# Kernel tuning notes

Measured on AMD Instinct MI355X. Metric: run time of the kernel, lower is better.

Reference implementation:

```python
import jax, jax.numpy as jnp
import numpy as np

GAMMA = 0.99
N_CODES = 1024  # module hardcodes self.N = 2**10

def setup_inputs() -> dict:
    key = jax.random.key(0)
    k1, k2, k3, k4 = jax.random.split(key, 4)
    B, D, S = 16, 256, 2048
    N_q = 8
    return {
        "data_object": jax.random.normal(k1, (B, D, S), dtype=jnp.float32),
        "codebooks": jax.random.normal(k2, (N_q, N_CODES, D), dtype=jnp.float32),
        "N_i": jax.random.uniform(k3, (N_q, N_CODES), dtype=jnp.float32),
        "m_i": jax.random.normal(k4, (N_q, N_CODES, D), dtype=jnp.float32),
    }

def reference(data_object, codebooks, N_i, m_i):
    # data_object: [b, D, s] -> y: [b, s, D]
    b, D, s = data_object.shape
    y = jnp.transpose(data_object, (0, 2, 1))

    def stage(carry, xs):
        residual, cur_y = carry          # [b, s, D] each
        W, Ni, mi = xs                   # [N, D], [N], [N, D]
        flat = residual.reshape(-1, D)   # [b*s, D]
        d2 = (jnp.sum(flat * flat, axis=-1, keepdims=True)
              + jnp.sum(W * W, axis=-1)[None, :]
              - 2.0 * flat @ W.T)
        idx = jnp.argmin(d2, axis=-1)    # [b*s]
        Q = W[idx].reshape(residual.shape)
        # EMA codebook statistics (bincount + index_add as segment sums)
        counts = jax.ops.segment_sum(jnp.ones(idx.shape, flat.dtype), idx, num_segments=N_CODES)
        vec = jax.ops.segment_sum(flat, idx, num_segments=N_CODES)
        new_N = Ni * GAMMA + counts * (1.0 - GAMMA)
        new_m = mi * GAMMA + vec * (1.0 - GAMMA)
        new_W = new_m / jnp.clip(new_N, 1e-8)[:, None]
        return (residual - Q, cur_y + Q), (idx.reshape(b, s), new_N, new_m, new_W)

    init = (y, jnp.zeros_like(y))
    (residual, cur_y), (indices, new_N, new_m, new_W) = jax.lax.scan(
        stage, init, (codebooks, N_i, m_i))

    # straight-through estimator + commitment loss
    logits = y + jax.lax.stop_gradient(cur_y - y)       # [b, s, D]
    commitment_loss = jnp.mean((jax.lax.stop_gradient(cur_y) - y) ** 2)
    logits = jnp.transpose(logits, (0, 2, 1))           # back to [b, D, s]
    return logits, commitment_loss, indices, new_N, new_m, new_W
```

## Files before the change

### kernel.cpp

```cpp
#include <hip/hip_runtime.h>
#include <hip/hip_bf16.h>


using f16   = _Float16;
using f16x4 = __attribute__((ext_vector_type(4))) _Float16;
using f16x8 = __attribute__((ext_vector_type(8))) _Float16;
using f32x4 = __attribute__((ext_vector_type(4))) float;

#define GAMMA_F 0.99f
#define OMG_F   0.01f
#define LO_SCALE 1024.0f
#define LO_INV   (1.0f/1024.0f)

__global__ void sentinel_kernel(float* out, float v){
  if (threadIdx.x == 0 && blockIdx.x == 0) out[0] = v;
}

__global__ __launch_bounds__(64) void rownorm_kernel(const float* __restrict__ X,
                                                     float* __restrict__ out, int rows){
  int r = blockIdx.x;
  if (r >= rows) return;
  int l = threadIdx.x;
  const float* x = X + (size_t)r * 256;
  float s = 0.f;
  #pragma unroll
  for (int i = 0; i < 4; i++){ float v = x[l + i*64]; s += v*v; }
  #pragma unroll
  for (int o = 32; o > 0; o >>= 1) s += __shfl_down(s, o, 64);
  if (l == 0) out[r] = s;
}

__global__ __launch_bounds__(64) void wsplit_kernel(const float* __restrict__ W,
                                                    f16* __restrict__ frag){
  int blk = blockIdx.x;
  int lane = threadIdx.x;
  int code = (blk >> 3 << 4) + (lane & 15);
  int k0   = (blk & 7)*32 + (lane >> 4)*8;
  const float* src = W + (size_t)code * 256 + k0;
  float4 a = *(const float4*)(src);
  float4 b = *(const float4*)(src + 4);
  float x[8] = {a.x,a.y,a.z,a.w, b.x,b.y,b.z,b.w};
  f16x8 h8, l8;
  #pragma unroll
  for (int i = 0; i < 8; i++){
    f16 h = (f16)x[i];
    h8[i] = h;
    l8[i] = (f16)((x[i] - (float)h) * LO_SCALE);
  }
  f16* dst = frag + (size_t)blk * 1024 + lane*8;
  *(f16x8*)dst         = h8;
  *(f16x8*)(dst + 512) = l8;
}

__global__ __launch_bounds__(256) void init_kernel(const float* __restrict__ data,
                                                   f16* __restrict__ AH, f16* __restrict__ AL,
                                                   float* __restrict__ rnorm){
  __shared__ float rs[32][257];
  __shared__ float nrmp[32][8];
  int blk = blockIdx.x, b = blk >> 6, s0 = (blk & 63) * 32;
  int tid = threadIdx.x, c = tid & 31, g = tid >> 5;
  const float* dptr = data + (size_t)b * 524288 + s0;
  float np_ = 0.f;
  #pragma unroll 8
  for (int dd = 0; dd < 32; ++dd){
    int d = g*32 + dd;
    float x = dptr[(size_t)d * 2048 + c];
    rs[c][d] = x;
    np_ += x*x;
  }
  nrmp[c][g] = np_;
  __syncthreads();
  if (tid < 32){
    float s = 0.f;
    #pragma unroll
    for (int gg = 0; gg < 8; ++gg) s += nrmp[tid][gg];
    rnorm[blk*32 + tid] = s;
  }
  int r0 = blk*32;
  int c2 = tid >> 3, k0 = (tid & 7) * 32;
  #pragma unroll
  for (int jc = 0; jc < 4; ++jc){
    f16x8 h8, l8;
    #pragma unroll
    for (int j = 0; j < 8; ++j){
      float x = rs[c2][k0 + jc*8 + j];
      f16 h = (f16)x;
      h8[j] = h;
      l8[j] = (f16)((x - (float)h) * LO_SCALE);
    }
    size_t off = (size_t)(r0 + c2) * 256 + k0 + jc*8;
    *(f16x8*)(AH + off) = h8;
    *(f16x8*)(AL + off) = l8;
  }
}

__global__ __launch_bounds__(256) void out4init_kernel(const float* __restrict__ mi,
                                                       float* __restrict__ out4){
  int e4 = blockIdx.x*256 + threadIdx.x;
  float4 v = ((const float4*)mi)[e4];
  v.x *= GAMMA_F; v.y *= GAMMA_F; v.z *= GAMMA_F; v.w *= GAMMA_F;
  ((float4*)out4)[e4] = v;
}

__global__ __launch_bounds__(256, 2) void dist_kernel(
    const f16* __restrict__ AH, const f16* __restrict__ AL,
    const f16* __restrict__ whl, const float* __restrict__ wnorm,
    const float* __restrict__ rnorm, float* __restrict__ pv,
    unsigned short* __restrict__ pi, int q)
{
  __shared__ f16 Bs[2][8192];
  const int tid = threadIdx.x;
  const int lane = tid & 63;
  const int w = tid >> 6;
  const int rb = blockIdx.x, cs = blockIdx.y;
  const int rlo = lane & 15, kg = lane >> 4;
  const int T0 = rb*8 + w*2;

  f16x8 aH[2][8], aL[2][8];
  #pragma unroll
  for (int rt = 0; rt < 2; ++rt)
    #pragma unroll
    for (int kf = 0; kf < 8; ++kf){
      size_t off = (size_t)((T0+rt)*16 + rlo) * 256 + kf*32 + kg*8;
      aH[rt][kf] = *(const f16x8*)(AH + off);
      aL[rt][kf] = *(const f16x8*)(AL + off);
    }
  float rn[2][4];
  #pragma unroll
  for (int rt = 0; rt < 2; ++rt)
    #pragma unroll
    for (int i = 0; i < 4; ++i)
      rn[rt][i] = rnorm[(T0+rt)*16 + kg*4 + i];

  const f16* wb = whl + (size_t)q * 64 * 8192;
  const float* wn = wnorm + (q << 10);
  const int ct0 = cs * 16;

  float bestv[8]; int besti[8];
  #pragma unroll
  for (int r8 = 0; r8 < 8; ++r8){ bestv[r8] = 3.4e38f; besti[r8] = 0; }

  {
    const f16* src = wb + (size_t)ct0 * 8192;
    f16x8 st[4];
    #pragma unroll
    for (int j = 0; j < 4; ++j) st[j] = *(const f16x8*)(src + tid*8 + j*2048);
    #pragma unroll
    for (int j = 0; j < 4; ++j) *(f16x8*)(&Bs[0][0] + tid*8 + j*2048) = st[j];
  }

  for (int it = 0; it < 16; ++it){
    int ct = ct0 + it;
    __syncthreads();
    f16x8 nx[4];
    if (it < 15){
      const f16* src = wb + (size_t)(ct+1) * 8192;
      #pragma unroll
      for (int j = 0; j < 4; ++j) nx[j] = *(const f16x8*)(src + tid*8 + j*2048);
    }
    const f16* bb = &Bs[it & 1][0];
    f32x4 hh[2], cr[2];
    #pragma unroll
    for (int rt = 0; rt < 2; ++rt){ hh[rt] = (f32x4)0.0f; cr[rt] = (f32x4)0.0f; }
    #pragma unroll
    for (int kf = 0; kf < 8; ++kf){
      f16x8 bh = *(const f16x8*)(bb + kf*1024 + lane*8);
      f16x8 bl = *(const f16x8*)(bb + kf*1024 + 512 + lane*8);
      hh[0] = __builtin_amdgcn_mfma_f32_16x16x32_f16(aH[0][kf], bh, hh[0], 0,0,0);
      cr[0] = __builtin_amdgcn_mfma_f32_16x16x32_f16(aH[0][kf], bl, cr[0], 0,0,0);
      cr[0] = __builtin_amdgcn_mfma_f32_16x16x32_f16(aL[0][kf], bh, cr[0], 0,0,0);
      hh[1] = __builtin_amdgcn_mfma_f32_16x16x32_f16(aH[1][kf], bh, hh[1], 0,0,0);
      cr[1] = __builtin_amdgcn_mfma_f32_16x16x32_f16(aH[1][kf], bl, cr[1], 0,0,0);
      cr[1] = __builtin_amdgcn_mfma_f32_16x16x32_f16(aL[1][kf], bh, cr[1], 0,0,0);
    }
    {
      int code = (ct << 4) + rlo;
      float wnc = wn[code];
      #pragma unroll
      for (int rt = 0; rt < 2; ++rt)
        #pragma unroll
        for (int i = 0; i < 4; ++i){
          float dot = hh[rt][i] + cr[rt][i] * LO_INV;
          float d2 = (rn[rt][i] + wnc) - 2.0f * dot;
          int r8 = rt*4 + i;
          if (d2 < bestv[r8] || (d2 == bestv[r8] && code < besti[r8])){
            bestv[r8] = d2; besti[r8] = code;
          }
        }
    }
    if (it < 15){
      #pragma unroll
      for (int j = 0; j < 4; ++j) *(f16x8*)(&Bs[(it+1) & 1][0] + tid*8 + j*2048) = nx[j];
    }
  }

  #pragma unroll
  for (int off = 1; off <= 8; off <<= 1){
    #pragma unroll
    for (int r8 = 0; r8 < 8; ++r8){
      float ov = __shfl_xor(bestv[r8], off, 16);
      int   oi = __shfl_xor(besti[r8], off, 16);
      if (ov < bestv[r8] || (ov == bestv[r8] && oi < besti[r8])){
        bestv[r8] = ov; besti[r8] = oi;
      }
    }
  }
  if (rlo == 0){
    #pragma unroll
    for (int r8 = 0; r8 < 8; ++r8){
      int rt = r8 >> 2, i = r8 & 3;
      int grow = (T0 + rt)*16 + kg*4 + i;
      pv[cs*32768 + grow] = bestv[r8];
      pi[cs*32768 + grow] = (unsigned short)besti[r8];
    }
  }
}

__global__ __launch_bounds__(256) void combine_kernel(
    const float* __restrict__ pv, const unsigned short* __restrict__ pi,
    float* __restrict__ out2q, unsigned short* __restrict__ blockhist){
  __shared__ int h[1024];
  int tid = threadIdx.x, b = blockIdx.x;
  #pragma unroll
  for (int i = 0; i < 4; ++i) h[tid + 256*i] = 0;
  __syncthreads();
  #pragma unroll
  for (int j = 0; j < 4; ++j){
    int row = b*1024 + tid + 256*j;
    float bv = pv[row]; int bi = pi[row];
    #pragma unroll
    for (int cs = 1; cs < 4; ++cs){
      float v = pv[cs*32768 + row];
      int  ii = pi[cs*32768 + row];
      if (v < bv){ bv = v; bi = ii; }
    }
    out2q[row] = (float)bi;
    atomicAdd(&h[bi], 1);
  }
  __syncthreads();
  #pragma unroll
  for (int i = 0; i < 4; ++i)
    blockhist[b*1024 + tid + 256*i] = (unsigned short)h[tid + 256*i];
}

__global__ __launch_bounds__(256) void scan_kernel(unsigned short* __restrict__ blockhist,
                                                   const float* __restrict__ Ni,
                                                   float* __restrict__ out3, int q){
  __shared__ int wtot[4];
  int tid = threadIdx.x, lane = tid & 63, w = tid >> 6;
  ushort4* bh4 = (ushort4*)blockhist;
  int tx=0, ty=0, tz=0, tw=0;
  for (int b = 0; b < 32; ++b){
    ushort4 h = bh4[b*256 + tid];
    tx += h.x; ty += h.y; tz += h.z; tw += h.w;
  }
  int s = tx + ty + tz + tw;
  int v = s;
  #pragma unroll
  for (int d = 1; d < 64; d <<= 1){
    int o = __shfl_up(v, d, 64);
    if (lane >= d) v += o;
  }
  if (lane == 63) wtot[w] = v;
  __syncthreads();
  int woff = 0;
  #pragma unroll
  for (int ww = 0; ww < 4; ++ww) if (ww < w) woff += wtot[ww];
  int base = woff + v - s;
  const int qb = q << 10;
  out3[qb + tid*4+0] = Ni[qb + tid*4+0]*GAMMA_F + (float)tx*OMG_F;
  out3[qb + tid*4+1] = Ni[qb + tid*4+1]*GAMMA_F + (float)ty*OMG_F;
  out3[qb + tid*4+2] = Ni[qb + tid*4+2]*GAMMA_F + (float)tz*OMG_F;
  out3[qb + tid*4+3] = Ni[qb + tid*4+3]*GAMMA_F + (float)tw*OMG_F;
  int r0 = base, r1 = base + tx, r2 = r1 + ty, r3 = r2 + tz;
  for (int b = 0; b < 32; ++b){
    ushort4 h = bh4[b*256 + tid];
    ushort4 st; st.x = (unsigned short)r0; st.y = (unsigned short)r1;
    st.z = (unsigned short)r2; st.w = (unsigned short)r3;
    bh4[b*256 + tid] = st;
    r0 += h.x; r1 += h.y; r2 += h.z; r3 += h.w;
  }
}

__global__ __launch_bounds__(256) void scatter_kernel(const float* __restrict__ out2q,
                                                      const unsigned short* __restrict__ blockhist,
                                                      unsigned short* __restrict__ rowlist){
  __shared__ int cur[1024];
  int tid = threadIdx.x, b = blockIdx.x;
  #pragma unroll
  for (int i = 0; i < 4; ++i) cur[tid + 256*i] = blockhist[b*1024 + tid + 256*i];
  __syncthreads();
  #pragma unroll
  for (int j = 0; j < 4; ++j){
    int row = b*1024 + tid + 256*j;
    int c = (int)out2q[row];
    int pos = atomicAdd(&cur[c], 1);
    rowlist[pos] = (unsigned short)row;
  }
}

__global__ __launch_bounds__(64) void update_kernel(
    f16* __restrict__ AH, f16* __restrict__ AL,
    const unsigned short* __restrict__ rowlist, const float* __restrict__ out2q,
    const float* __restrict__ codebooks, float* __restrict__ out4,
    float* __restrict__ rnorm, int q)
{
  const int lane = threadIdx.x;
  const int s0 = blockIdx.x * 16;
  int myrow = 0, mycode = 0;
  if (lane < 16){
    myrow = rowlist[s0 + lane];
    mycode = (int)out2q[myrow];
  }
  float vs[4] = {0.f, 0.f, 0.f, 0.f};
  float Wk[4] = {0.f, 0.f, 0.f, 0.f};
  int prev = -1;
  for (int s = 0; s < 16; ++s){
    int row  = __shfl(myrow, s, 64);
    int code = __shfl(mycode, s, 64);
    if (code != prev){
      if (prev >= 0){
        float* dst = out4 + (((size_t)q << 10) + prev)*256 + lane*4;
        #pragma unroll
        for (int t = 0; t < 4; ++t) atomicAdd(dst + t, vs[t] * OMG_F);
      }
      float4 wv = *(const float4*)&codebooks[(((size_t)q << 10) + code)*256 + lane*4];
      Wk[0] = wv.x; Wk[1] = wv.y; Wk[2] = wv.z; Wk[3] = wv.w;
      vs[0] = vs[1] = vs[2] = vs[3] = 0.f;
      prev = code;
    }
    size_t base = (size_t)row * 256 + lane*4;
    f16x4 h4 = *(const f16x4*)(AH + base);
    f16x4 l4 = *(const f16x4*)(AL + base);
    f16x4 nh, nl;
    float p = 0.f;
    #pragma unroll
    for (int t = 0; t < 4; ++t){
      float rj = (float)h4[t] + (float)l4[t] * LO_INV;
      vs[t] += rj;
      float rn_ = rj - Wk[t];
      f16 hh = (f16)rn_;
      nh[t] = hh;
      nl[t] = (f16)((rn_ - (float)hh) * LO_SCALE);
      p += rn_ * rn_;
    }
    *(f16x4*)(AH + base) = nh;
    *(f16x4*)(AL + base) = nl;
    #pragma unroll
    for (int o = 32; o > 0; o >>= 1) p += __shfl_down(p, o, 64);
    if (lane == 0) rnorm[row] = p;
  }
  if (prev >= 0){
    float* dst = out4 + (((size_t)q << 10) + prev)*256 + lane*4;
    #pragma unroll
    for (int t = 0; t < 4; ++t) atomicAdd(dst + t, vs[t] * OMG_F);
  }
}

__global__ __launch_bounds__(256) void logits_loss_kernel(
    const float* __restrict__ data, const f16* __restrict__ AH, const f16* __restrict__ AL,
    float* __restrict__ out0, float* __restrict__ out1)
{
  __shared__ float rs[32][257];
  int blk = blockIdx.x, b = blk >> 6, s0 = (blk & 63) * 32;
  int tid = threadIdx.x;
  int r0 = blk*32;
  int c2 = tid >> 3, k0 = (tid & 7) * 32;
  #pragma unroll
  for (int jc = 0; jc < 4; ++jc){
    size_t off = (size_t)(r0 + c2) * 256 + k0 + jc*8;
    f16x8 h8 = *(const f16x8*)(AH + off);
    f16x8 l8 = *(const f16x8*)(AL + off);
    #pragma unroll
    for (int j = 0; j < 8; ++j)
      rs[c2][k0 + jc*8 + j] = (float)h8[j] + (float)l8[j] * LO_INV;
  }
  __syncthreads();
  int c = tid & 31, g = tid >> 5;
  const float* dptr = data + (size_t)b * 524288 + s0;
  float* optr = out0 + (size_t)b * 524288 + s0;
  float lsum = 0.f;
  #pragma unroll 8
  for (int dd = 0; dd < 32; ++dd){
    int d = g*32 + dd;
    float r = rs[c][d];
    lsum += r*r;
    optr[(size_t)d * 2048 + c] = dptr[(size_t)d * 2048 + c] - r;
  }
  #pragma unroll
  for (int o = 32; o > 0; o >>= 1) lsum += __shfl_down(lsum, o, 64);
  if ((tid & 63) == 0) atomicAdd(out1, lsum * (1.0f / 8388608.0f));
}

__global__ __launch_bounds__(256) void out5_kernel(const float* __restrict__ out4,
                                                   const float* __restrict__ out3,
                                                   float* __restrict__ out5){
  int e4 = blockIdx.x*256 + threadIdx.x;
  float Nn = fmaxf(out3[e4 >> 6], 1e-8f);
  float4 v = ((const float4*)out4)[e4];
  v.x /= Nn; v.y /= Nn; v.z /= Nn; v.w /= Nn;
  ((float4*)out5)[e4] = v;
}

extern "C" void kernel_launch(void* const* d_in, const int* in_sizes, int n_in,
                              void* d_out, int out_size, void* d_ws, size_t ws_size,
                              hipStream_t stream){
  float* out = (float*)d_out;

  const float* data = nullptr; const float* codebooks = nullptr;
  const float* Ni = nullptr;   const float* mi = nullptr;
  for (int i = 0; i < n_in; ++i){
    if      (in_sizes[i] == 8388608) data = (const float*)d_in[i];
    else if (in_sizes[i] == 8192)    Ni   = (const float*)d_in[i];
    else if (in_sizes[i] == 2097152){
      if (!codebooks) codebooks = (const float*)d_in[i];
      else            mi        = (const float*)d_in[i];
    }
  }
  if (!data || !codebooks || !Ni || !mi){
    sentinel_kernel<<<1, 64, 0, stream>>>(out, 6666.0f);
    return;
  }

  const size_t ws_need = 43122688ull;
  if (ws_size < ws_need){
    sentinel_kernel<<<1, 64, 0, stream>>>(out, 7777.0f);
    return;
  }
  f16*   AH     = (f16*)d_ws;
  f16*   AL     = AH + 8388608;
  f16*   whl    = AL + 8388608;
  float* wnormb = (float*)(whl + 4194304);
  float* rnorm  = wnormb + 8192;
  unsigned short* blockhist = (unsigned short*)(rnorm + 32768);
  unsigned short* rowlist   = blockhist + 32768;
  float* pv     = (float*)(rowlist + 32768);
  unsigned short* pi = (unsigned short*)(pv + 131072);

  float* out0 = out;
  float* out1 = out0 + 8388608;
  float* out2 = out1 + 1;
  float* out3 = out2 + 262144;
  float* out4 = out3 + 8192;
  float* out5 = out4 + 2097152;

  hipMemsetAsync(out1, 0, sizeof(float), stream);

  wsplit_kernel<<<dim3(4096), 64, 0, stream>>>(codebooks, whl);
  rownorm_kernel<<<dim3(8192), 64, 0, stream>>>(codebooks, wnormb, 8192);
  init_kernel<<<dim3(1024), 256, 0, stream>>>(data, AH, AL, rnorm);
  out4init_kernel<<<dim3(2048), 256, 0, stream>>>(mi, out4);

  for (int q = 0; q < 8; ++q){
    float* out2q = out2 + (size_t)q * 32768;
    dist_kernel<<<dim3(256, 4), 256, 0, stream>>>(AH, AL, whl, wnormb, rnorm, pv, pi, q);
    combine_kernel<<<dim3(32), 256, 0, stream>>>(pv, pi, out2q, blockhist);
    scan_kernel<<<dim3(1), 256, 0, stream>>>(blockhist, Ni, out3, q);
    scatter_kernel<<<dim3(32), 256, 0, stream>>>(out2q, blockhist, rowlist);
    update_kernel<<<dim3(2048), 64, 0, stream>>>(AH, AL, rowlist, out2q,
                                                 codebooks, out4, rnorm, q);
  }

  logits_loss_kernel<<<dim3(1024), 256, 0, stream>>>(data, AH, AL, out0, out1);
  out5_kernel<<<dim3(2048), 256, 0, stream>>>(out4, out3, out5);
}
```

Before: 867.0 us.

## Load codebook low-half fragments from global into registers and prefetch update rows

In the distance kernel, only the high-half codebook fragments are now staged in shared memory, which halves the LDS footprint. The low-half fragments are loaded straight from global memory into registers on each tile iteration. In the update kernel, the next row's residual halves are loaded one step ahead, so their latency overlaps with the current row's work. The aims are to cut LDS traffic, raise occupancy and hide load latency, at the cost of more global loads and extra register pressure in the distance kernel.

New measurement: 1.022 ms. 17.9% more time.

```diff
diff --git a/kernel.cpp b/kernel.cpp
--- a/kernel.cpp
+++ b/kernel.cpp
@@ -108,7 +108,7 @@
     const float* __restrict__ rnorm, float* __restrict__ pv,
     unsigned short* __restrict__ pi, int q)
 {
-  __shared__ f16 Bs[2][8192];
+  __shared__ f16 Bs[2][4096];
   const int tid = threadIdx.x;
   const int lane = tid & 63;
   const int w = tid >> 6;
@@ -132,7 +132,7 @@
     for (int i = 0; i < 4; ++i)
       rn[rt][i] = rnorm[(T0+rt)*16 + kg*4 + i];
 
-  const f16* wb = whl + (size_t)q * 64 * 8192;
+  const f16* wb = whl + (size_t)q * 524288;
   const float* wn = wnorm + (q << 10);
   const int ct0 = cs * 16;
 
@@ -141,22 +141,28 @@
   for (int r8 = 0; r8 < 8; ++r8){ bestv[r8] = 3.4e38f; besti[r8] = 0; }
 
   {
-    const f16* src = wb + (size_t)ct0 * 8192;
-    f16x8 st[4];
-    #pragma unroll
-    for (int j = 0; j < 4; ++j) st[j] = *(const f16x8*)(src + tid*8 + j*2048);
-    #pragma unroll
-    for (int j = 0; j < 4; ++j) *(f16x8*)(&Bs[0][0] + tid*8 + j*2048) = st[j];
+    const f16* src = wb + (size_t)ct0*8192 + (w*2)*1024 + lane*8;
+    f16x8 s0 = *(const f16x8*)(src);
+    f16x8 s1 = *(const f16x8*)(src + 1024);
+    f16* dst = &Bs[0][0] + (w*2)*512 + lane*8;
+    *(f16x8*)dst         = s0;
+    *(f16x8*)(dst + 512) = s1;
   }
 
   for (int it = 0; it < 16; ++it){
     int ct = ct0 + it;
     __syncthreads();
-    f16x8 nx[4];
+    f16x8 nx0, nx1;
     if (it < 15){
-      const f16* src = wb + (size_t)(ct+1) * 8192;
+      const f16* src = wb + (size_t)(ct+1)*8192 + (w*2)*1024 + lane*8;
+      nx0 = *(const f16x8*)(src);
+      nx1 = *(const f16x8*)(src + 1024);
+    }
+    f16x8 blr[8];
+    {
+      const f16* bls = wb + (size_t)ct*8192 + 512 + lane*8;
       #pragma unroll
-      for (int j = 0; j < 4; ++j) nx[j] = *(const f16x8*)(src + tid*8 + j*2048);
+      for (int kf = 0; kf < 8; ++kf) blr[kf] = *(const f16x8*)(bls + kf*1024);
     }
     const f16* bb = &Bs[it & 1][0];
     f32x4 hh[2], cr[2];
@@ -164,14 +170,13 @@
     for (int rt = 0; rt < 2; ++rt){ hh[rt] = (f32x4)0.0f; cr[rt] = (f32x4)0.0f; }
     #pragma unroll
     for (int kf = 0; kf < 8; ++kf){
-      f16x8 bh = *(const f16x8*)(bb + kf*1024 + lane*8);
-      f16x8 bl = *(const f16x8*)(bb + kf*1024 + 512 + lane*8);
-      hh[0] = __builtin_amdgcn_mfma_f32_16x16x32_f16(aH[0][kf], bh, hh[0], 0,0,0);
-      cr[0] = __builtin_amdgcn_mfma_f32_16x16x32_f16(aH[0][kf], bl, cr[0], 0,0,0);
-      cr[0] = __builtin_amdgcn_mfma_f32_16x16x32_f16(aL[0][kf], bh, cr[0], 0,0,0);
-      hh[1] = __builtin_amdgcn_mfma_f32_16x16x32_f16(aH[1][kf], bh, hh[1], 0,0,0);
-      cr[1] = __builtin_amdgcn_mfma_f32_16x16x32_f16(aH[1][kf], bl, cr[1], 0,0,0);
-      cr[1] = __builtin_amdgcn_mfma_f32_16x16x32_f16(aL[1][kf], bh, cr[1], 0,0,0);
+      f16x8 bh = *(const f16x8*)(bb + kf*512 + lane*8);
+      hh[0] = __builtin_amdgcn_mfma_f32_16x16x32_f16(aH[0][kf], bh,      hh[0], 0,0,0);
+      cr[0] = __builtin_amdgcn_mfma_f32_16x16x32_f16(aH[0][kf], blr[kf], cr[0], 0,0,0);
+      cr[0] = __builtin_amdgcn_mfma_f32_16x16x32_f16(aL[0][kf], bh,      cr[0], 0,0,0);
+      hh[1] = __builtin_amdgcn_mfma_f32_16x16x32_f16(aH[1][kf], bh,      hh[1], 0,0,0);
+      cr[1] = __builtin_amdgcn_mfma_f32_16x16x32_f16(aH[1][kf], blr[kf], cr[1], 0,0,0);
+      cr[1] = __builtin_amdgcn_mfma_f32_16x16x32_f16(aL[1][kf], bh,      cr[1], 0,0,0);
     }
     {
       int code = (ct << 4) + rlo;
@@ -189,8 +194,9 @@
         }
     }
     if (it < 15){
-      #pragma unroll
-      for (int j = 0; j < 4; ++j) *(f16x8*)(&Bs[(it+1) & 1][0] + tid*8 + j*2048) = nx[j];
+      f16* dst = &Bs[(it+1) & 1][0] + (w*2)*512 + lane*8;
+      *(f16x8*)dst         = nx0;
+      *(f16x8*)(dst + 512) = nx1;
     }
   }
 
@@ -315,9 +321,18 @@
   float vs[4] = {0.f, 0.f, 0.f, 0.f};
   float Wk[4] = {0.f, 0.f, 0.f, 0.f};
   int prev = -1;
+  int rowp = __shfl(myrow, 0, 64);
+  f16x4 ph = *(const f16x4*)(AH + (size_t)rowp*256 + lane*4);
+  f16x4 pl = *(const f16x4*)(AL + (size_t)rowp*256 + lane*4);
   for (int s = 0; s < 16; ++s){
     int row  = __shfl(myrow, s, 64);
     int code = __shfl(mycode, s, 64);
+    f16x4 h4 = ph, l4 = pl;
+    if (s < 15){
+      int rown = __shfl(myrow, s+1, 64);
+      ph = *(const f16x4*)(AH + (size_t)rown*256 + lane*4);
+      pl = *(const f16x4*)(AL + (size_t)rown*256 + lane*4);
+    }
     if (code != prev){
       if (prev >= 0){
         float* dst = out4 + (((size_t)q << 10) + prev)*256 + lane*4;
@@ -330,8 +345,6 @@
       prev = code;
     }
     size_t base = (size_t)row * 256 + lane*4;
-    f16x4 h4 = *(const f16x4*)(AH + base);
-    f16x4 l4 = *(const f16x4*)(AL + base);
     f16x4 nh, nl;
     float p = 0.f;
     #pragma unroll
```

## Merge argmin partials via 64-bit atomicMin, fuse scan with scatter, deepen dist tiles

Applied to the files above, without the earlier changes.

The dist kernel now packs each row's best distance and code into an order-preserving 64-bit key and merges the four column-split partials with atomicMin. This replaces the separate pv/pi buffers and the combine pass, and the hist kernel resets the key buffer after reading it. The single-block scan and the scatter kernel are merged into one 32-block kernel, so each block recomputes the prefix totals itself. The dist kernel also stages two code tiles per iteration, doubling its LDS use, and raises wave priority around the MFMA loop. The update kernel prefetches the next row's residual. Together these remove one launch per stage and some latency, at the cost of atomic contention, redundant scan work and higher LDS pressure.

Measured after the change: 904.7 us. 4.3% more time.

```diff
diff --git a/kernel.cpp b/kernel.cpp
--- a/kernel.cpp
+++ b/kernel.cpp
@@ -6,6 +6,7 @@
 using f16x4 = __attribute__((ext_vector_type(4))) _Float16;
 using f16x8 = __attribute__((ext_vector_type(8))) _Float16;
 using f32x4 = __attribute__((ext_vector_type(4))) float;
+typedef unsigned long long u64;
 
 #define GAMMA_F 0.99f
 #define OMG_F   0.01f
@@ -105,10 +106,9 @@
 __global__ __launch_bounds__(256, 2) void dist_kernel(
     const f16* __restrict__ AH, const f16* __restrict__ AL,
     const f16* __restrict__ whl, const float* __restrict__ wnorm,
-    const float* __restrict__ rnorm, float* __restrict__ pv,
-    unsigned short* __restrict__ pi, int q)
+    const float* __restrict__ rnorm, u64* __restrict__ keybuf, int q)
 {
-  __shared__ f16 Bs[2][8192];
+  __shared__ f16 Bs[2][16384];
   const int tid = threadIdx.x;
   const int lane = tid & 63;
   const int w = tid >> 6;
@@ -132,49 +132,52 @@
     for (int i = 0; i < 4; ++i)
       rn[rt][i] = rnorm[(T0+rt)*16 + kg*4 + i];
 
-  const f16* wb = whl + (size_t)q * 64 * 8192;
+  const f16* wb = whl + (size_t)q * 524288;
   const float* wn = wnorm + (q << 10);
   const int ct0 = cs * 16;
 
   float bestv[8]; int besti[8];
   #pragma unroll
-  for (int r8 = 0; r8 < 8; ++r8){ bestv[r8] = 3.4e38f; besti[r8] = 0; }
+  for (int r8_ = 0; r8_ < 8; ++r8_){ bestv[r8_] = 3.4e38f; besti[r8_] = 0; }
 
   {
     const f16* src = wb + (size_t)ct0 * 8192;
-    f16x8 st[4];
-    #pragma unroll
-    for (int j = 0; j < 4; ++j) st[j] = *(const f16x8*)(src + tid*8 + j*2048);
-    #pragma unroll
-    for (int j = 0; j < 4; ++j) *(f16x8*)(&Bs[0][0] + tid*8 + j*2048) = st[j];
-  }
-
-  for (int it = 0; it < 16; ++it){
-    int ct = ct0 + it;
+    f16x8 st[8];
+    #pragma unroll
+    for (int j = 0; j < 8; ++j) st[j] = *(const f16x8*)(src + tid*8 + j*2048);
+    #pragma unroll
+    for (int j = 0; j < 8; ++j) *(f16x8*)(&Bs[0][0] + tid*8 + j*2048) = st[j];
+  }
+
+  for (int it = 0; it < 8; ++it){
+    int cb = ct0 + it*2;
     __syncthreads();
-    f16x8 nx[4];
-    if (it < 15){
-      const f16* src = wb + (size_t)(ct+1) * 8192;
+    f16x8 nx[8];
+    if (it < 7){
+      const f16* src = wb + (size_t)(cb+2) * 8192;
       #pragma unroll
-      for (int j = 0; j < 4; ++j) nx[j] = *(const f16x8*)(src + tid*8 + j*2048);
-    }
-    const f16* bb = &Bs[it & 1][0];
-    f32x4 hh[2], cr[2];
-    #pragma unroll
-    for (int rt = 0; rt < 2; ++rt){ hh[rt] = (f32x4)0.0f; cr[rt] = (f32x4)0.0f; }
-    #pragma unroll
-    for (int kf = 0; kf < 8; ++kf){
-      f16x8 bh = *(const f16x8*)(bb + kf*1024 + lane*8);
-      f16x8 bl = *(const f16x8*)(bb + kf*1024 + 512 + lane*8);
-      hh[0] = __builtin_amdgcn_mfma_f32_16x16x32_f16(aH[0][kf], bh, hh[0], 0,0,0);
-      cr[0] = __builtin_amdgcn_mfma_f32_16x16x32_f16(aH[0][kf], bl, cr[0], 0,0,0);
-      cr[0] = __builtin_amdgcn_mfma_f32_16x16x32_f16(aL[0][kf], bh, cr[0], 0,0,0);
-      hh[1] = __builtin_amdgcn_mfma_f32_16x16x32_f16(aH[1][kf], bh, hh[1], 0,0,0);
-      cr[1] = __builtin_amdgcn_mfma_f32_16x16x32_f16(aH[1][kf], bl, cr[1], 0,0,0);
-      cr[1] = __builtin_amdgcn_mfma_f32_16x16x32_f16(aL[1][kf], bh, cr[1], 0,0,0);
-    }
-    {
-      int code = (ct << 4) + rlo;
+      for (int j = 0; j < 8; ++j) nx[j] = *(const f16x8*)(src + tid*8 + j*2048);
+    }
+    #pragma unroll
+    for (int sub = 0; sub < 2; ++sub){
+      const f16* bb = &Bs[it & 1][0] + sub*8192;
+      f32x4 hh[2], cr[2];
+      #pragma unroll
+      for (int rt = 0; rt < 2; ++rt){ hh[rt] = (f32x4)0.0f; cr[rt] = (f32x4)0.0f; }
+      __builtin_amdgcn_s_setprio(1);
+      #pragma unroll
+      for (int kf = 0; kf < 8; ++kf){
+        f16x8 bh = *(const f16x8*)(bb + kf*1024 + lane*8);
+        f16x8 bl = *(const f16x8*)(bb + kf*1024 + 512 + lane*8);
+        hh[0] = __builtin_amdgcn_mfma_f32_16x16x32_f16(aH[0][kf], bh, hh[0], 0,0,0);
+        cr[0] = __builtin_amdgcn_mfma_f32_16x16x32_f16(aH[0][kf], bl, cr[0], 0,0,0);
+        cr[0] = __builtin_amdgcn_mfma_f32_16x16x32_f16(aL[0][kf], bh, cr[0], 0,0,0);
+        hh[1] = __builtin_amdgcn_mfma_f32_16x16x32_f16(aH[1][kf], bh, hh[1], 0,0,0);
+        cr[1] = __builtin_amdgcn_mfma_f32_16x16x32_f16(aH[1][kf], bl, cr[1], 0,0,0);
+        cr[1] = __builtin_amdgcn_mfma_f32_16x16x32_f16(aL[1][kf], bh, cr[1], 0,0,0);
+      }
+      __builtin_amdgcn_s_setprio(0);
+      int code = ((cb + sub) << 4) + rlo;
       float wnc = wn[code];
       #pragma unroll
       for (int rt = 0; rt < 2; ++rt)
@@ -182,43 +185,45 @@
         for (int i = 0; i < 4; ++i){
           float dot = hh[rt][i] + cr[rt][i] * LO_INV;
           float d2 = (rn[rt][i] + wnc) - 2.0f * dot;
-          int r8 = rt*4 + i;
-          if (d2 < bestv[r8] || (d2 == bestv[r8] && code < besti[r8])){
-            bestv[r8] = d2; besti[r8] = code;
+          int r8_ = rt*4 + i;
+          if (d2 < bestv[r8_] || (d2 == bestv[r8_] && code < besti[r8_])){
+            bestv[r8_] = d2; besti[r8_] = code;
           }
         }
     }
-    if (it < 15){
+    if (it < 7){
       #pragma unroll
-      for (int j = 0; j < 4; ++j) *(f16x8*)(&Bs[(it+1) & 1][0] + tid*8 + j*2048) = nx[j];
+      for (int j = 0; j < 8; ++j) *(f16x8*)(&Bs[(it+1) & 1][0] + tid*8 + j*2048) = nx[j];
     }
   }
 
   #pragma unroll
   for (int off = 1; off <= 8; off <<= 1){
     #pragma unroll
-    for (int r8 = 0; r8 < 8; ++r8){
-      float ov = __shfl_xor(bestv[r8], off, 16);
-      int   oi = __shfl_xor(besti[r8], off, 16);
-      if (ov < bestv[r8] || (ov == bestv[r8] && oi < besti[r8])){
-        bestv[r8] = ov; besti[r8] = oi;
+    for (int r8_ = 0; r8_ < 8; ++r8_){
+      float ov = __shfl_xor(bestv[r8_], off, 16);
+      int   oi = __shfl_xor(besti[r8_], off, 16);
+      if (ov < bestv[r8_] || (ov == bestv[r8_] && oi < besti[r8_])){
+        bestv[r8_] = ov; besti[r8_] = oi;
       }
     }
   }
   if (rlo == 0){
     #pragma unroll
-    for (int r8 = 0; r8 < 8; ++r8){
-      int rt = r8 >> 2, i = r8 & 3;
+    for (int r8_ = 0; r8_ < 8; ++r8_){
+      int rt = r8_ >> 2, i = r8_ & 3;
       int grow = (T0 + rt)*16 + kg*4 + i;
-      pv[cs*32768 + grow] = bestv[r8];
-      pi[cs*32768 + grow] = (unsigned short)besti[r8];
-    }
-  }
-}
-
-__global__ __launch_bounds__(256) void combine_kernel(
-    const float* __restrict__ pv, const unsigned short* __restrict__ pi,
-    float* __restrict__ out2q, unsigned short* __restrict__ blockhist){
+      unsigned fb = __float_as_uint(bestv[r8_]);
+      fb = (fb & 0x80000000u) ? ~fb : (fb | 0x80000000u);
+      u64 key = ((u64)fb << 32) | (unsigned)besti[r8_];
+      atomicMin(keybuf + grow, key);
+    }
+  }
+}
+
+__global__ __launch_bounds__(256) void hist_kernel(u64* __restrict__ keybuf,
+                                                   float* __restrict__ out2q,
+                                                   unsigned short* __restrict__ blockhist){
   __shared__ int h[1024];
   int tid = threadIdx.x, b = blockIdx.x;
   #pragma unroll
@@ -227,15 +232,11 @@
   #pragma unroll
   for (int j = 0; j < 4; ++j){
     int row = b*1024 + tid + 256*j;
-    float bv = pv[row]; int bi = pi[row];
-    #pragma unroll
-    for (int cs = 1; cs < 4; ++cs){
-      float v = pv[cs*32768 + row];
-      int  ii = pi[cs*32768 + row];
-      if (v < bv){ bv = v; bi = ii; }
-    }
-    out2q[row] = (float)bi;
-    atomicAdd(&h[bi], 1);
+    u64 k = keybuf[row];
+    keybuf[row] = ~0ull;
+    int c = (int)(k & 0xFFFF);
+    out2q[row] = (float)c;
+    atomicAdd(&h[c], 1);
   }
   __syncthreads();
   #pragma unroll
@@ -243,18 +244,22 @@
     blockhist[b*1024 + tid + 256*i] = (unsigned short)h[tid + 256*i];
 }
 
-__global__ __launch_bounds__(256) void scan_kernel(unsigned short* __restrict__ blockhist,
-                                                   const float* __restrict__ Ni,
-                                                   float* __restrict__ out3, int q){
+__global__ __launch_bounds__(256) void scanscatter_kernel(
+    const unsigned short* __restrict__ blockhist, const float* __restrict__ out2q,
+    unsigned short* __restrict__ rowlist, const float* __restrict__ Ni,
+    float* __restrict__ out3, int q)
+{
   __shared__ int wtot[4];
-  int tid = threadIdx.x, lane = tid & 63, w = tid >> 6;
-  ushort4* bh4 = (ushort4*)blockhist;
-  int tx=0, ty=0, tz=0, tw=0;
-  for (int b = 0; b < 32; ++b){
-    ushort4 h = bh4[b*256 + tid];
-    tx += h.x; ty += h.y; tz += h.z; tw += h.w;
-  }
-  int s = tx + ty + tz + tw;
+  __shared__ int cur[1024];
+  int tid = threadIdx.x, b = blockIdx.x, lane = tid & 63, w = tid >> 6;
+  const ushort4* bh4 = (const ushort4*)blockhist;
+  int tot[4] = {0,0,0,0}, pre[4] = {0,0,0,0};
+  for (int bb = 0; bb < 32; ++bb){
+    ushort4 h = bh4[bb*256 + tid];
+    if (bb < b){ pre[0]+=h.x; pre[1]+=h.y; pre[2]+=h.z; pre[3]+=h.w; }
+    tot[0]+=h.x; tot[1]+=h.y; tot[2]+=h.z; tot[3]+=h.w;
+  }
+  int s = tot[0]+tot[1]+tot[2]+tot[3];
   int v = s;
   #pragma unroll
   for (int d = 1; d < 64; d <<= 1){
@@ -267,28 +272,17 @@
   #pragma unroll
   for (int ww = 0; ww < 4; ++ww) if (ww < w) woff += wtot[ww];
   int base = woff + v - s;
-  const int qb = q << 10;
-  out3[qb + tid*4+0] = Ni[qb + tid*4+0]*GAMMA_F + (float)tx*OMG_F;
-  out3[qb + tid*4+1] = Ni[qb + tid*4+1]*GAMMA_F + (float)ty*OMG_F;
-  out3[qb + tid*4+2] = Ni[qb + tid*4+2]*GAMMA_F + (float)tz*OMG_F;
-  out3[qb + tid*4+3] = Ni[qb + tid*4+3]*GAMMA_F + (float)tw*OMG_F;
-  int r0 = base, r1 = base + tx, r2 = r1 + ty, r3 = r2 + tz;
-  for (int b = 0; b < 32; ++b){
-    ushort4 h = bh4[b*256 + tid];
-    ushort4 st; st.x = (unsigned short)r0; st.y = (unsigned short)r1;
-    st.z = (unsigned short)r2; st.w = (unsigned short)r3;
-    bh4[b*256 + tid] = st;
-    r0 += h.x; r1 += h.y; r2 += h.z; r3 += h.w;
-  }
-}
-
-__global__ __launch_bounds__(256) void scatter_kernel(const float* __restrict__ out2q,
-                                                      const unsigned short* __restrict__ blockhist,
-                                                      unsigned short* __restrict__ rowlist){
-  __shared__ int cur[1024];
-  int tid = threadIdx.x, b = blockIdx.x;
-  #pragma unroll
-  for (int i = 0; i < 4; ++i) cur[tid + 256*i] = blockhist[b*1024 + tid + 256*i];
+  if (b == 0){
+    const int qb = q << 10;
+    out3[qb + 4*tid+0] = Ni[qb + 4*tid+0]*GAMMA_F + (float)tot[0]*OMG_F;
+    out3[qb + 4*tid+1] = Ni[qb + 4*tid+1]*GAMMA_F + (float)tot[1]*OMG_F;
+    out3[qb + 4*tid+2] = Ni[qb + 4*tid+2]*GAMMA_F + (float)tot[2]*OMG_F;
+    out3[qb + 4*tid+3] = Ni[qb + 4*tid+3]*GAMMA_F + (float)tot[3]*OMG_F;
+  }
+  cur[4*tid+0] = base + pre[0];
+  cur[4*tid+1] = base + tot[0] + pre[1];
+  cur[4*tid+2] = base + tot[0]+tot[1] + pre[2];
+  cur[4*tid+3] = base + tot[0]+tot[1]+tot[2] + pre[3];
   __syncthreads();
   #pragma unroll
   for (int j = 0; j < 4; ++j){
@@ -315,9 +309,18 @@
   float vs[4] = {0.f, 0.f, 0.f, 0.f};
   float Wk[4] = {0.f, 0.f, 0.f, 0.f};
   int prev = -1;
+  int rowp = __shfl(myrow, 0, 64);
+  f16x4 ph = *(const f16x4*)(AH + (size_t)rowp*256 + lane*4);
+  f16x4 pl = *(const f16x4*)(AL + (size_t)rowp*256 + lane*4);
   for (int s = 0; s < 16; ++s){
     int row  = __shfl(myrow, s, 64);
     int code = __shfl(mycode, s, 64);
+    f16x4 h4 = ph, l4 = pl;
+    if (s < 15){
+      int rown = __shfl(myrow, s+1, 64);
+      ph = *(const f16x4*)(AH + (size_t)rown*256 + lane*4);
+      pl = *(const f16x4*)(AL + (size_t)rown*256 + lane*4);
+    }
     if (code != prev){
       if (prev >= 0){
         float* dst = out4 + (((size_t)q << 10) + prev)*256 + lane*4;
@@ -330,8 +333,6 @@
       prev = code;
     }
     size_t base = (size_t)row * 256 + lane*4;
-    f16x4 h4 = *(const f16x4*)(AH + base);
-    f16x4 l4 = *(const f16x4*)(AL + base);
     f16x4 nh, nl;
     float p = 0.f;
     #pragma unroll
@@ -422,7 +423,7 @@
     return;
   }
 
-  const size_t ws_need = 43122688ull;
+  const size_t ws_need = 42500096ull;
   if (ws_size < ws_need){
     sentinel_kernel<<<1, 64, 0, stream>>>(out, 7777.0f);
     return;
@@ -434,8 +435,7 @@
   float* rnorm  = wnormb + 8192;
   unsigned short* blockhist = (unsigned short*)(rnorm + 32768);
   unsigned short* rowlist   = blockhist + 32768;
-  float* pv     = (float*)(rowlist + 32768);
-  unsigned short* pi = (unsigned short*)(pv + 131072);
+  u64*   keybuf = (u64*)(rowlist + 32768);
 
   float* out0 = out;
   float* out1 = out0 + 8388608;
@@ -445,6 +445,7 @@
   float* out5 = out4 + 2097152;
 
   hipMemsetAsync(out1, 0, sizeof(float), stream);
+  hipMemsetAsync(keybuf, 0xFF, 262144, stream);
 
   wsplit_kernel<<<dim3(4096), 64, 0, stream>>>(codebooks, whl);
   rownorm_kernel<<<dim3(8192), 64, 0, stream>>>(codebooks, wnormb, 8192);
@@ -453,10 +454,10 @@
 
   for (int q = 0; q < 8; ++q){
     float* out2q = out2 + (size_t)q * 32768;
-    dist_kernel<<<dim3(256, 4), 256, 0, stream>>>(AH, AL, whl, wnormb, rnorm, pv, pi, q);
-    combine_kernel<<<dim3(32), 256, 0, stream>>>(pv, pi, out2q, blockhist);
-    scan_kernel<<<dim3(1), 256, 0, stream>>>(blockhist, Ni, out3, q);
-    scatter_kernel<<<dim3(32), 256, 0, stream>>>(out2q, blockhist, rowlist);
+    dist_kernel<<<dim3(256, 4), 256, 0, stream>>>(AH, AL, whl, wnormb, rnorm, keybuf, q);
+    hist_kernel<<<dim3(32), 256, 0, stream>>>(keybuf, out2q, blockhist);
+    scanscatter_kernel<<<dim3(32), 256, 0, stream>>>(blockhist, out2q, rowlist,
+                                                     Ni, out3, q);
     update_kernel<<<dim3(2048), 64, 0, stream>>>(AH, AL, rowlist, out2q,
                                                  codebooks, out4, rnorm, q);
   }
```
